# Kernel optimization log

Measured on AMD Instinct MI355X. Metric: run time of the kernel, lower is better.

The kernel has to match this reference:

```python
import jax, jax.numpy as jnp
import numpy as np

N_GO, N_KE, D = 8000, 2000, 16
N_LAYERS, N_TISSUE, DRUG = 3, 512, 2048
B = 256


def _scatter_add(msgs, dst, n):
    # msgs: [B, E, D] -> [B, n, D], summing messages into destination nodes
    Bm, _, d = msgs.shape
    return jnp.zeros((Bm, n, d), msgs.dtype).at[:, dst, :].add(msgs)


def setup_inputs() -> dict:
    key = jax.random.key(0)
    ks = jax.random.split(key, 20)
    inp = {
        "x": jax.random.normal(ks[0], (B, N_GO + DRUG), jnp.float32),
        "go_ke_src": jax.random.randint(ks[1], (50000,), 0, N_GO),
        "go_ke_dst": jax.random.randint(ks[2], (50000,), 0, N_KE),
        "ke_ke_src": jax.random.randint(ks[3], (20000,), 0, N_KE),
        "ke_ke_dst": jax.random.randint(ks[4], (20000,), 0, N_KE),
        "tissue": jax.random.randint(ks[5], (N_TISSUE,), 0, N_KE),
    }
    def w(k, shape, fan_in):
        return jax.random.normal(k, shape, jnp.float32) / np.sqrt(fan_in)
    inp["W_dec"] = w(ks[6], (N_GO, D), 1.0)          # per-GO scalar->vector layer
    inp["b_dec"] = jnp.zeros((N_GO, D), jnp.float32)
    inp["W_g2k"] = w(ks[7], (D, D), D)
    inp["b_g2k"] = jnp.zeros((D,), jnp.float32)
    inp["W_kk"] = w(ks[8], (N_LAYERS, D, D), D)
    inp["b_kk"] = jnp.zeros((N_LAYERS, D), jnp.float32)
    inp["w_ke"] = w(ks[9], (D,), D)                   # node readout D->1
    inp["b_ke"] = jnp.zeros((), jnp.float32)
    inp["W_bio1"] = w(ks[10], (N_TISSUE, 256), N_TISSUE)
    inp["b_bio1"] = jnp.zeros((256,), jnp.float32)
    inp["W_bio2"] = w(ks[11], (256, 128), 256)
    inp["b_bio2"] = jnp.zeros((128,), jnp.float32)
    inp["W_drug1"] = w(ks[12], (DRUG, 512), DRUG)
    inp["b_drug1"] = jnp.zeros((512,), jnp.float32)
    inp["W_drug2"] = w(ks[13], (512, 128), 512)
    inp["b_drug2"] = jnp.zeros((128,), jnp.float32)
    inp["W_pred"] = w(ks[14], (256, 1), 256)
    inp["b_pred"] = jnp.zeros((1,), jnp.float32)
    return inp


def reference(x, go_ke_src, go_ke_dst, ke_ke_src, ke_ke_dst, tissue,
              W_dec, b_dec, W_g2k, b_g2k, W_kk, b_kk, w_ke, b_ke,
              W_bio1, b_bio1, W_bio2, b_bio2,
              W_drug1, b_drug1, W_drug2, b_drug2, W_pred, b_pred):
    # go_decode_layer: per-GO scalar -> D-dim node feature
    go = jnp.tanh(x[:, :-DRUG, None] * W_dec + b_dec)          # [B, N_GO, D]
    # go2ke: gather source GO features, scatter-add into KE nodes, transform
    ke = _scatter_add(go[:, go_ke_src, :], go_ke_dst, N_KE)    # [B, N_KE, D]
    ke = jnp.tanh(ke @ W_g2k + b_g2k)
    # ke2ke message-passing layers
    for l in range(W_kk.shape[0]):
        agg = _scatter_add(ke[:, ke_ke_src, :], ke_ke_dst, N_KE)
        ke = jnp.tanh((ke + agg) @ W_kk[l] + b_kk[l])
    # ke_layer: per-node readout D -> scalar
    ke = jnp.tanh(jnp.einsum('bnd,d->bn', ke, w_ke) + b_ke)    # [B, N_KE]
    # tissue gather + bio MLP head
    bio = ke[:, tissue]                                         # [B, N_TISSUE]
    bio = jax.nn.relu(bio @ W_bio1 + b_bio1)
    bio = jax.nn.relu(bio @ W_bio2 + b_bio2)
    # drug fingerprint MLP head
    drug = x[:, -DRUG:]
    drug = jax.nn.relu(drug @ W_drug1 + b_drug1)
    drug = jax.nn.relu(drug @ W_drug2 + b_drug2)
    # predictor on concatenated features
    comb = jnp.concatenate([bio, drug], axis=-1)                # [B, 256]
    return comb @ W_pred + b_pred                               # [B, 1]
```

## Files before the change

### kernel.cpp

```cpp
#include <hip/hip_runtime.h>
#include <hip/hip_bf16.h>
#include <cstdint>
#include <cstddef>

#define BATCH 256
#define NGO   8000
#define NKE   2000
#define DD    16
#define XCOLS 10048
#define NDRUG 2048
#define NT    512
#define NSLAB 8
#define SB    32
#define TANH_SCALE 2.885390081777926f

__device__ __forceinline__ float tanh_fast(float z) {
    float e = __builtin_amdgcn_exp2f(z * TANH_SCALE);
    float r = __builtin_amdgcn_rcpf(e + 1.0f);
    return fmaf(-2.0f, r, 1.0f);
}

__device__ __forceinline__ float rcp_core(float zp) {
    float e = __builtin_amdgcn_exp2f(zp);
    return __builtin_amdgcn_rcpf(e + 1.0f);
}

__device__ __forceinline__ void add4(float4& a, const float4 b) {
    a.x += b.x; a.y += b.y; a.z += b.z; a.w += b.w;
}

#define RFL(v) __builtin_amdgcn_readfirstlane(v)

__global__ void k_scan2(const int* __restrict__ cnt_go, const int* __restrict__ cnt_kk,
                        int* __restrict__ rp_go, int* __restrict__ rp_kk) {
    const int* cnt = blockIdx.x ? cnt_kk : cnt_go;
    int* rowptr    = blockIdx.x ? rp_kk  : rp_go;
    __shared__ int s[2048];
    int t = threadIdx.x;
    s[t]        = (t        < NKE) ? cnt[t]        : 0;
    s[t + 1024] = (t + 1024 < NKE) ? cnt[t + 1024] : 0;
    __syncthreads();
    for (int st = 1; st < 2048; st <<= 1) {
        int v0 = (t >= st) ? s[t - st] : 0;
        int v1 = s[t + 1024 - st];
        __syncthreads();
        s[t] += v0; s[t + 1024] += v1;
        __syncthreads();
    }
    if (t == 0) rowptr[0] = 0;
    rowptr[t + 1] = s[t];
    if (t + 1024 < NKE) rowptr[t + 1025] = s[t + 1024];
}

__global__ void k_fill2(const int* __restrict__ gs, const int* __restrict__ gdst,
                        const int* __restrict__ ks, const int* __restrict__ kdst,
                        int Eg, int Ek,
                        const int* __restrict__ rp_go, int* __restrict__ cur_go, int* __restrict__ col_go,
                        const int* __restrict__ rp_kk, int* __restrict__ cur_kk, int* __restrict__ col_kk) {
    int e = blockIdx.x * 256 + threadIdx.x;
    if (e < Eg) {
        int d = gdst[e];
        int p = atomicAdd(&cur_go[d], 1);
        col_go[rp_go[d] + p] = gs[e];
    } else if (e < Eg + Ek) {
        int e2 = e - Eg;
        int d = kdst[e2];
        int p = atomicAdd(&cur_kk[d], 1);
        col_kk[rp_kk[d] + p] = ks[e2];
    }
}

__global__ __launch_bounds__(256) void k_prep(const float* __restrict__ x,
                                              float* __restrict__ xT,
                                              float* __restrict__ xdT,
                                              const float* __restrict__ bd,
                                              float* __restrict__ bds,
                                              const int* __restrict__ gdst,
                                              const int* __restrict__ kdst,
                                              int* __restrict__ cnt_go,
                                              int* __restrict__ cnt_kk,
                                              int Eg, int Ek) {
    int bid = blockIdx.x;
    if (bid >= 1128) {
        int e = (bid - 1128) * 256 + threadIdx.x;
        if (e < Eg) atomicAdd(&cnt_go[gdst[e]], 1);
        else if (e < Eg + Ek) atomicAdd(&cnt_kk[kdst[e - Eg]], 1);
        return;
    }
    if (bid >= 628) {
        int i = (bid - 628) * 256 + threadIdx.x;
        bds[i] = bd[i] * TANH_SCALE;
        return;
    }
    __shared__ float tile[64][69];
    int c4 = threadIdx.x & 15, rr = threadIdx.x >> 4;
    int n0, b0;
    bool isgo = bid < 500;
    if (isgo) { n0 = (bid % 125) * 64; b0 = (bid / 125) * 64; }
    else      { int t = bid - 500; n0 = NGO + (t & 31) * 64; b0 = (t >> 5) * 64; }
#pragma unroll
    for (int i = 0; i < 4; i++) {
        int row = rr + i * 16;
        float4 v = *(const float4*)&x[(size_t)(b0 + row) * XCOLS + n0 + c4 * 4];
        tile[row][c4 * 4 + 0] = v.x; tile[row][c4 * 4 + 1] = v.y;
        tile[row][c4 * 4 + 2] = v.z; tile[row][c4 * 4 + 3] = v.w;
    }
    __syncthreads();
#pragma unroll
    for (int i = 0; i < 4; i++) {
        int nrow = rr + i * 16;
        float4 w;
        w.x = tile[c4 * 4 + 0][nrow]; w.y = tile[c4 * 4 + 1][nrow];
        w.z = tile[c4 * 4 + 2][nrow]; w.w = tile[c4 * 4 + 3][nrow];
        if (isgo) {
            w.x *= TANH_SCALE; w.y *= TANH_SCALE; w.z *= TANH_SCALE; w.w *= TANH_SCALE;
            *(float4*)&xT[(size_t)(n0 + nrow) * 256 + b0 + c4 * 4] = w;
        } else {
            *(float4*)&xdT[(size_t)(n0 - NGO + nrow) * 256 + b0 + c4 * 4] = w;
        }
    }
}

__global__ __launch_bounds__(128) void k_fuse(const float* __restrict__ xT,
                                              const int* __restrict__ rowptr,
                                              const int* __restrict__ col,
                                              const float* __restrict__ Wd,
                                              const float* __restrict__ bds,
                                              const float* __restrict__ W,
                                              const float* __restrict__ bias,
                                              float* __restrict__ ke) {
    __shared__ float pre[32 * 17];
    __shared__ float Ws[256];
    __shared__ float bs[16];
    int s = blockIdx.x & 7, n = blockIdx.x >> 3;
    int tid = threadIdx.x;
    Ws[tid] = W[tid]; Ws[tid + 128] = W[tid + 128];
    if (tid < 16) bs[tid] = bias[tid];
    int bloc = tid >> 2, d4 = tid & 3;
    int bglob = s * SB + bloc;

    int e   = RFL(rowptr[n]);
    int end = RFL(rowptr[n + 1]);
    float degF = (float)(end - e);
    float4 acc = make_float4(0, 0, 0, 0);
    for (; e + 3 < end; e += 4) {
        int s0 = RFL(col[e]);
        int s1 = RFL(col[e + 1]);
        int s2 = RFL(col[e + 2]);
        int s3 = RFL(col[e + 3]);
        float xv0 = (xT + (size_t)s0 * 256)[bglob];
        float xv1 = (xT + (size_t)s1 * 256)[bglob];
        float xv2 = (xT + (size_t)s2 * 256)[bglob];
        float xv3 = (xT + (size_t)s3 * 256)[bglob];
        float4 w0 = *(const float4*)(Wd  + (size_t)s0 * 16 + d4 * 4);
        float4 w1 = *(const float4*)(Wd  + (size_t)s1 * 16 + d4 * 4);
        float4 w2 = *(const float4*)(Wd  + (size_t)s2 * 16 + d4 * 4);
        float4 w3 = *(const float4*)(Wd  + (size_t)s3 * 16 + d4 * 4);
        float4 c0 = *(const float4*)(bds + (size_t)s0 * 16 + d4 * 4);
        float4 c1 = *(const float4*)(bds + (size_t)s1 * 16 + d4 * 4);
        float4 c2 = *(const float4*)(bds + (size_t)s2 * 16 + d4 * 4);
        float4 c3 = *(const float4*)(bds + (size_t)s3 * 16 + d4 * 4);
        acc.x += rcp_core(fmaf(xv0, w0.x, c0.x)) + rcp_core(fmaf(xv1, w1.x, c1.x))
               + rcp_core(fmaf(xv2, w2.x, c2.x)) + rcp_core(fmaf(xv3, w3.x, c3.x));
        acc.y += rcp_core(fmaf(xv0, w0.y, c0.y)) + rcp_core(fmaf(xv1, w1.y, c1.y))
               + rcp_core(fmaf(xv2, w2.y, c2.y)) + rcp_core(fmaf(xv3, w3.y, c3.y));
        acc.z += rcp_core(fmaf(xv0, w0.z, c0.z)) + rcp_core(fmaf(xv1, w1.z, c1.z))
               + rcp_core(fmaf(xv2, w2.z, c2.z)) + rcp_core(fmaf(xv3, w3.z, c3.z));
        acc.w += rcp_core(fmaf(xv0, w0.w, c0.w)) + rcp_core(fmaf(xv1, w1.w, c1.w))
               + rcp_core(fmaf(xv2, w2.w, c2.w)) + rcp_core(fmaf(xv3, w3.w, c3.w));
    }
    for (; e < end; ++e) {
        int s0 = RFL(col[e]);
        float xv0 = (xT + (size_t)s0 * 256)[bglob];
        float4 w0 = *(const float4*)(Wd  + (size_t)s0 * 16 + d4 * 4);
        float4 c0 = *(const float4*)(bds + (size_t)s0 * 16 + d4 * 4);
        acc.x += rcp_core(fmaf(xv0, w0.x, c0.x));
        acc.y += rcp_core(fmaf(xv0, w0.y, c0.y));
        acc.z += rcp_core(fmaf(xv0, w0.z, c0.z));
        acc.w += rcp_core(fmaf(xv0, w0.w, c0.w));
    }
    pre[bloc * 17 + d4 * 4 + 0] = fmaf(-2.0f, acc.x, degF);
    pre[bloc * 17 + d4 * 4 + 1] = fmaf(-2.0f, acc.y, degF);
    pre[bloc * 17 + d4 * 4 + 2] = fmaf(-2.0f, acc.z, degF);
    pre[bloc * 17 + d4 * 4 + 3] = fmaf(-2.0f, acc.w, degF);
    __syncthreads();

    float4 o;
    float* op = &o.x;
#pragma unroll
    for (int q = 0; q < 4; q++) {
        int dp = d4 * 4 + q;
        float a = bs[dp];
#pragma unroll
        for (int d = 0; d < 16; d++) a = fmaf(pre[bloc * 17 + d], Ws[d * 16 + dp], a);
        op[q] = tanh_fast(a);
    }
    *(float4*)&ke[((size_t)s * NKE + n) * 512 + bloc * 16 + d4 * 4] = o;
}

__global__ __launch_bounds__(128) void k_layer(const float* __restrict__ kin,
                                               const int* __restrict__ rowptr,
                                               const int* __restrict__ col,
                                               const float* __restrict__ W,
                                               const float* __restrict__ bias,
                                               float* __restrict__ kout) {
    __shared__ float pre[32 * 17];
    __shared__ float Ws[256];
    __shared__ float bs[16];
    int s = blockIdx.x & 7, n = blockIdx.x >> 3;
    int tid = threadIdx.x;
    Ws[tid] = W[tid]; Ws[tid + 128] = W[tid + 128];
    if (tid < 16) bs[tid] = bias[tid];
    int bloc = tid >> 2, d4 = tid & 3;
    const float* slab = kin + (size_t)s * NKE * 512;

    float4 acc = *(const float4*)(slab + (size_t)n * 512 + tid * 4);
    int e   = RFL(rowptr[n]);
    int end = RFL(rowptr[n + 1]);
    for (; e + 3 < end; e += 4) {
        int c0 = RFL(col[e]), c1 = RFL(col[e + 1]), c2 = RFL(col[e + 2]), c3 = RFL(col[e + 3]);
        float4 v0 = *(const float4*)(slab + (size_t)c0 * 512 + tid * 4);
        float4 v1 = *(const float4*)(slab + (size_t)c1 * 512 + tid * 4);
        float4 v2 = *(const float4*)(slab + (size_t)c2 * 512 + tid * 4);
        float4 v3 = *(const float4*)(slab + (size_t)c3 * 512 + tid * 4);
        add4(acc, v0); add4(acc, v1); add4(acc, v2); add4(acc, v3);
    }
    for (; e < end; ++e) {
        int c0 = RFL(col[e]);
        float4 v0 = *(const float4*)(slab + (size_t)c0 * 512 + tid * 4);
        add4(acc, v0);
    }
    pre[bloc * 17 + d4 * 4 + 0] = acc.x;
    pre[bloc * 17 + d4 * 4 + 1] = acc.y;
    pre[bloc * 17 + d4 * 4 + 2] = acc.z;
    pre[bloc * 17 + d4 * 4 + 3] = acc.w;
    __syncthreads();

    float4 o;
    float* op = &o.x;
#pragma unroll
    for (int q = 0; q < 4; q++) {
        int dp = d4 * 4 + q;
        float a = bs[dp];
#pragma unroll
        for (int d = 0; d < 16; d++) a = fmaf(pre[bloc * 17 + d], Ws[d * 16 + dp], a);
        op[q] = tanh_fast(a);
    }
    *(float4*)&kout[(size_t)s * NKE * 512 + (size_t)n * 512 + bloc * 16 + d4 * 4] = o;
}

__device__ __forceinline__ void dev_kescalar(int t, const float* __restrict__ ke,
                                             const int* __restrict__ tissue,
                                             const float* __restrict__ wke,
                                             const float* __restrict__ bke,
                                             float* __restrict__ bioT) {
    int b = threadIdx.x;
    int n = RFL(tissue[t]);
    int s = b >> 5, bloc = b & 31;
    const float4* kp = (const float4*)&ke[((size_t)s * NKE + n) * 512 + bloc * 16];
    const float4* wp = (const float4*)wke;
    float4 k0 = kp[0], k1 = kp[1], k2 = kp[2], k3 = kp[3];
    float4 w0 = wp[0], w1 = wp[1], w2 = wp[2], w3 = wp[3];
    float acc = bke[0];
    acc += k0.x * w0.x + k0.y * w0.y + k0.z * w0.z + k0.w * w0.w;
    acc += k1.x * w1.x + k1.y * w1.y + k1.z * w1.z + k1.w * w1.w;
    acc += k2.x * w2.x + k2.y * w2.y + k2.z * w2.z + k2.w * w2.w;
    acc += k3.x * w3.x + k3.y * w3.y + k3.z * w3.z + k3.w * w3.w;
    bioT[t * 256 + b] = tanh_fast(acc);
}

__device__ __forceinline__ void dev_gemm(int bid, const float* __restrict__ A,
                                         const float* __restrict__ W,
                                         float* __restrict__ Cpart,
                                         int N, int Kper, int gx,
                                         float (*As)[68], float (*Ws)[68]) {
    int tid = threadIdx.x;
    int tx = tid & 15, ty = tid >> 4;
    int jx = bid % gx;
    int by = (bid / gx) & 3;
    int ks = bid / (gx * 4);
    int jt = jx * 64, bt = by * 64;
    int k0 = ks * Kper;

    float acc[4][4];
#pragma unroll
    for (int i = 0; i < 4; i++)
#pragma unroll
        for (int j = 0; j < 4; j++) acc[i][j] = 0.0f;

    for (int kc = 0; kc < Kper; kc += 32) {
#pragma unroll
        for (int i = 0; i < 8; i++) {
            int idx = tid + i * 256;
            int kk = idx >> 6, cc = idx & 63;
            As[kk][cc] = A[(size_t)(k0 + kc + kk) * 256 + bt + cc];
            Ws[kk][cc] = W[(size_t)(k0 + kc + kk) * N + jt + cc];
        }
        __syncthreads();
#pragma unroll 8
        for (int kk = 0; kk < 32; kk++) {
            float4 a = *(const float4*)&As[kk][tx * 4];
            float4 w = *(const float4*)&Ws[kk][ty * 4];
            acc[0][0] = fmaf(w.x, a.x, acc[0][0]); acc[0][1] = fmaf(w.x, a.y, acc[0][1]);
            acc[0][2] = fmaf(w.x, a.z, acc[0][2]); acc[0][3] = fmaf(w.x, a.w, acc[0][3]);
            acc[1][0] = fmaf(w.y, a.x, acc[1][0]); acc[1][1] = fmaf(w.y, a.y, acc[1][1]);
            acc[1][2] = fmaf(w.y, a.z, acc[1][2]); acc[1][3] = fmaf(w.y, a.w, acc[1][3]);
            acc[2][0] = fmaf(w.z, a.x, acc[2][0]); acc[2][1] = fmaf(w.z, a.y, acc[2][1]);
            acc[2][2] = fmaf(w.z, a.z, acc[2][2]); acc[2][3] = fmaf(w.z, a.w, acc[2][3]);
            acc[3][0] = fmaf(w.w, a.x, acc[3][0]); acc[3][1] = fmaf(w.w, a.y, acc[3][1]);
            acc[3][2] = fmaf(w.w, a.z, acc[3][2]); acc[3][3] = fmaf(w.w, a.w, acc[3][3]);
        }
        __syncthreads();
    }
#pragma unroll
    for (int jy = 0; jy < 4; jy++) {
        int j = jt + ty * 4 + jy;
        float4 v = make_float4(acc[jy][0], acc[jy][1], acc[jy][2], acc[jy][3]);
        *(float4*)&Cpart[((size_t)ks * N + j) * 256 + bt + tx * 4] = v;
    }
}

__device__ __forceinline__ void dev_red(int j, const float* __restrict__ Cpart,
                                        const float* __restrict__ bias,
                                        float* __restrict__ C, int N, int S) {
    int b = threadIdx.x;
    float acc = bias[j];
    for (int s = 0; s < S; s++) acc += Cpart[((size_t)s * N + j) * 256 + b];
    C[j * 256 + b] = fmaxf(acc, 0.0f);
}

__global__ __launch_bounds__(256) void k_kg(const float* __restrict__ ke,
                                            const int* __restrict__ tissue,
                                            const float* __restrict__ wke,
                                            const float* __restrict__ bke,
                                            float* __restrict__ bioT,
                                            const float* __restrict__ A,
                                            const float* __restrict__ W,
                                            float* __restrict__ Cpart,
                                            int N, int Kper, int gx, int nk) {
    __shared__ float As[32][68];
    __shared__ float Ws[32][68];
    int bid = blockIdx.x;
    if (bid < nk) dev_kescalar(bid, ke, tissue, wke, bke, bioT);
    else          dev_gemm(bid - nk, A, W, Cpart, N, Kper, gx, As, Ws);
}

__global__ __launch_bounds__(256) void k_gr(const float* __restrict__ A,
                                            const float* __restrict__ W,
                                            float* __restrict__ Cpart,
                                            int N, int Kper, int gx, int gB,
                                            const float* __restrict__ Rcp,
                                            const float* __restrict__ Rbias,
                                            float* __restrict__ RC, int RN, int RS) {
    __shared__ float As[32][68];
    __shared__ float Ws[32][68];
    int bid = blockIdx.x;
    if (bid < gB) dev_gemm(bid, A, W, Cpart, N, Kper, gx, As, Ws);
    else          dev_red(bid - gB, Rcp, Rbias, RC, RN, RS);
}

__global__ __launch_bounds__(256) void k_red(const float* __restrict__ Cpart,
                                             const float* __restrict__ bias,
                                             float* __restrict__ C, int N, int S) {
    dev_red(blockIdx.x, Cpart, bias, C, N, S);
}

__global__ __launch_bounds__(256) void k_final(const float* __restrict__ bio2T,
                                               const float* __restrict__ drug2T,
                                               const float* __restrict__ Wp,
                                               const float* __restrict__ bp,
                                               float* __restrict__ out) {
    int b = threadIdx.x;
    float acc = bp[0];
#pragma unroll 8
    for (int i = 0; i < 128; i++) acc = fmaf(bio2T[i * 256 + b], Wp[i], acc);
#pragma unroll 8
    for (int i = 0; i < 128; i++) acc = fmaf(drug2T[i * 256 + b], Wp[128 + i], acc);
    out[b] = acc;
}

extern "C" void kernel_launch(void* const* d_in, const int* in_sizes, int n_in,
                              void* d_out, int out_size, void* d_ws, size_t ws_size,
                              hipStream_t stream) {
    const float* x       = (const float*)d_in[0];
    const int*   go_src  = (const int*)d_in[1];
    const int*   go_dst  = (const int*)d_in[2];
    const int*   kk_src  = (const int*)d_in[3];
    const int*   kk_dst  = (const int*)d_in[4];
    const int*   tissue  = (const int*)d_in[5];
    const float* W_dec   = (const float*)d_in[6];
    const float* b_dec   = (const float*)d_in[7];
    const float* W_g2k   = (const float*)d_in[8];
    const float* b_g2k   = (const float*)d_in[9];
    const float* W_kk    = (const float*)d_in[10];
    const float* b_kk    = (const float*)d_in[11];
    const float* w_ke    = (const float*)d_in[12];
    const float* b_ke    = (const float*)d_in[13];
    const float* W_bio1  = (const float*)d_in[14];
    const float* b_bio1  = (const float*)d_in[15];
    const float* W_bio2  = (const float*)d_in[16];
    const float* b_bio2  = (const float*)d_in[17];
    const float* W_drug1 = (const float*)d_in[18];
    const float* b_drug1 = (const float*)d_in[19];
    const float* W_drug2 = (const float*)d_in[20];
    const float* b_drug2 = (const float*)d_in[21];
    const float* W_pred  = (const float*)d_in[22];
    const float* b_pred  = (const float*)d_in[23];
    float* out = (float*)d_out;

    const int E_GO = in_sizes[1];
    const int E_KK = in_sizes[3];

    char* wsb = (char*)d_ws;
    size_t off = 0;
    float* xT      = (float*)(wsb + off); off += (size_t)NGO * 256 * 4;
    float* ke_a    = (float*)(wsb + off); off += (size_t)NSLAB * NKE * 512 * 4;
    float* ke_b    = (float*)(wsb + off); off += (size_t)NSLAB * NKE * 512 * 4;
    float* bio_inT = (float*)(wsb + off); off += (size_t)NT * 256 * 4;
    float* bio1T   = (float*)(wsb + off); off += (size_t)256 * 256 * 4;
    float* bio2T   = (float*)(wsb + off); off += (size_t)128 * 256 * 4;
    float* xdT     = (float*)(wsb + off); off += (size_t)NDRUG * 256 * 4;
    float* drug1T  = (float*)(wsb + off); off += (size_t)512 * 256 * 4;
    float* drug2T  = (float*)(wsb + off); off += (size_t)128 * 256 * 4;
    float* bds     = (float*)(wsb + off); off += (size_t)NGO * 16 * 4;
    float* cp_d1   = (float*)(wsb + off); off += (size_t)8 * 512 * 256 * 4;
    float* cp_b1   = (float*)(wsb + off); off += (size_t)8 * 256 * 256 * 4;
    float* cp_d2   = (float*)(wsb + off); off += (size_t)8 * 128 * 256 * 4;
    float* cp_b2   = (float*)(wsb + off); off += (size_t)8 * 128 * 256 * 4;
    int* cnt_go    = (int*)(wsb + off); off += 2048 * 4;
    int* cur_go    = (int*)(wsb + off); off += 2048 * 4;
    int* cnt_kk    = (int*)(wsb + off); off += 2048 * 4;
    int* cur_kk    = (int*)(wsb + off); off += 2048 * 4;
    int* rp_go     = (int*)(wsb + off); off += 2048 * 4;
    int* rp_kk     = (int*)(wsb + off); off += 2048 * 4;
    int* col_go    = (int*)(wsb + off); off += 50048 * 4;
    int* col_kk    = (int*)(wsb + off); off += 20048 * 4;

    hipMemsetAsync(cnt_go, 0, 4 * 2048 * 4, stream);

    int Etot = E_GO + E_KK;
    int histBlocks = (Etot + 255) / 256;

    k_prep<<<1128 + histBlocks, 256, 0, stream>>>(x, xT, xdT, b_dec, bds,
                                                  go_dst, kk_dst, cnt_go, cnt_kk, E_GO, E_KK);
    k_scan2<<<2, 1024, 0, stream>>>(cnt_go, cnt_kk, rp_go, rp_kk);
    k_fill2<<<histBlocks, 256, 0, stream>>>(go_src, go_dst, kk_src, kk_dst, E_GO, E_KK,
                                            rp_go, cur_go, col_go, rp_kk, cur_kk, col_kk);

    k_fuse<<<NKE * NSLAB, 128, 0, stream>>>(xT, rp_go, col_go, W_dec, bds, W_g2k, b_g2k, ke_a);
    k_layer<<<NKE * NSLAB, 128, 0, stream>>>(ke_a, rp_kk, col_kk, W_kk + 0 * 256, b_kk + 0 * 16, ke_b);
    k_layer<<<NKE * NSLAB, 128, 0, stream>>>(ke_b, rp_kk, col_kk, W_kk + 1 * 256, b_kk + 1 * 16, ke_a);
    k_layer<<<NKE * NSLAB, 128, 0, stream>>>(ke_a, rp_kk, col_kk, W_kk + 2 * 256, b_kk + 2 * 16, ke_b);

    k_kg<<<NT + 256, 256, 0, stream>>>(ke_b, tissue, w_ke, b_ke, bio_inT,
                                       xdT, W_drug1, cp_d1, 512, 256, 8, NT);
    k_gr<<<128 + 512, 256, 0, stream>>>(bio_inT, W_bio1, cp_b1, 256, 64, 4, 128,
                                        cp_d1, b_drug1, drug1T, 512, 8);
    k_gr<<<64 + 256, 256, 0, stream>>>(drug1T, W_drug2, cp_d2, 128, 64, 2, 64,
                                       cp_b1, b_bio1, bio1T, 256, 8);
    k_gr<<<64 + 128, 256, 0, stream>>>(bio1T, W_bio2, cp_b2, 128, 32, 2, 64,
                                       cp_d2, b_drug2, drug2T, 128, 8);
    k_red<<<128, 256, 0, stream>>>(cp_b2, b_bio2, bio2T, 128, 8);

    k_final<<<1, 256, 0, stream>>>(bio2T, drug2T, W_pred, b_pred, out);
}
```

Before: 222.1 us.

## Gather neighbor KE features in fp16 and pair sigmoid terms to share reciprocals

Each KE layer kernel now also writes an fp16 copy of its output, and the next layer gathers neighbor features from that half-width copy. This halves the bytes moved by the random neighbor gathers, while the self term still reads fp32. In the GO-to-KE kernel, two sigmoid-style terms are combined algebraically so that one reciprocal is computed per pair instead of two. The costs are an extra fp16 store per layer, reduced precision in the aggregated messages, and possible overflow in the product of two exponentials for large inputs.

```diff
diff --git a/kernel.cpp b/kernel.cpp
--- a/kernel.cpp
+++ b/kernel.cpp
@@ -13,6 +13,8 @@
 #define NSLAB 8
 #define SB    32
 #define TANH_SCALE 2.885390081777926f
+
+typedef __attribute__((ext_vector_type(4))) _Float16 half4;
 
 __device__ __forceinline__ float tanh_fast(float z) {
     float e = __builtin_amdgcn_exp2f(z * TANH_SCALE);
@@ -128,7 +130,8 @@
                                               const float* __restrict__ bds,
                                               const float* __restrict__ W,
                                               const float* __restrict__ bias,
-                                              float* __restrict__ ke) {
+                                              float* __restrict__ ke,
+                                              _Float16* __restrict__ keH) {
     __shared__ float pre[32 * 17];
     __shared__ float Ws[256];
     __shared__ float bs[16];
@@ -143,33 +146,45 @@
     int end = RFL(rowptr[n + 1]);
     float degF = (float)(end - e);
     float4 acc = make_float4(0, 0, 0, 0);
-    for (; e + 3 < end; e += 4) {
+    for (; e + 1 < end; e += 2) {
         int s0 = RFL(col[e]);
         int s1 = RFL(col[e + 1]);
-        int s2 = RFL(col[e + 2]);
-        int s3 = RFL(col[e + 3]);
         float xv0 = (xT + (size_t)s0 * 256)[bglob];
         float xv1 = (xT + (size_t)s1 * 256)[bglob];
-        float xv2 = (xT + (size_t)s2 * 256)[bglob];
-        float xv3 = (xT + (size_t)s3 * 256)[bglob];
         float4 w0 = *(const float4*)(Wd  + (size_t)s0 * 16 + d4 * 4);
+        float4 c0 = *(const float4*)(bds + (size_t)s0 * 16 + d4 * 4);
         float4 w1 = *(const float4*)(Wd  + (size_t)s1 * 16 + d4 * 4);
-        float4 w2 = *(const float4*)(Wd  + (size_t)s2 * 16 + d4 * 4);
-        float4 w3 = *(const float4*)(Wd  + (size_t)s3 * 16 + d4 * 4);
-        float4 c0 = *(const float4*)(bds + (size_t)s0 * 16 + d4 * 4);
         float4 c1 = *(const float4*)(bds + (size_t)s1 * 16 + d4 * 4);
-        float4 c2 = *(const float4*)(bds + (size_t)s2 * 16 + d4 * 4);
-        float4 c3 = *(const float4*)(bds + (size_t)s3 * 16 + d4 * 4);
-        acc.x += rcp_core(fmaf(xv0, w0.x, c0.x)) + rcp_core(fmaf(xv1, w1.x, c1.x))
-               + rcp_core(fmaf(xv2, w2.x, c2.x)) + rcp_core(fmaf(xv3, w3.x, c3.x));
-        acc.y += rcp_core(fmaf(xv0, w0.y, c0.y)) + rcp_core(fmaf(xv1, w1.y, c1.y))
-               + rcp_core(fmaf(xv2, w2.y, c2.y)) + rcp_core(fmaf(xv3, w3.y, c3.y));
-        acc.z += rcp_core(fmaf(xv0, w0.z, c0.z)) + rcp_core(fmaf(xv1, w1.z, c1.z))
-               + rcp_core(fmaf(xv2, w2.z, c2.z)) + rcp_core(fmaf(xv3, w3.z, c3.z));
-        acc.w += rcp_core(fmaf(xv0, w0.w, c0.w)) + rcp_core(fmaf(xv1, w1.w, c1.w))
-               + rcp_core(fmaf(xv2, w2.w, c2.w)) + rcp_core(fmaf(xv3, w3.w, c3.w));
-    }
-    for (; e < end; ++e) {
+        {
+            float e0x = __builtin_amdgcn_exp2f(fmaf(xv0, w0.x, c0.x));
+            float e1x = __builtin_amdgcn_exp2f(fmaf(xv1, w1.x, c1.x));
+            float sx = e0x + e1x;
+            float den = fmaf(e0x, e1x, sx + 1.0f);
+            acc.x = fmaf(sx + 2.0f, __builtin_amdgcn_rcpf(den), acc.x);
+        }
+        {
+            float e0x = __builtin_amdgcn_exp2f(fmaf(xv0, w0.y, c0.y));
+            float e1x = __builtin_amdgcn_exp2f(fmaf(xv1, w1.y, c1.y));
+            float sx = e0x + e1x;
+            float den = fmaf(e0x, e1x, sx + 1.0f);
+            acc.y = fmaf(sx + 2.0f, __builtin_amdgcn_rcpf(den), acc.y);
+        }
+        {
+            float e0x = __builtin_amdgcn_exp2f(fmaf(xv0, w0.z, c0.z));
+            float e1x = __builtin_amdgcn_exp2f(fmaf(xv1, w1.z, c1.z));
+            float sx = e0x + e1x;
+            float den = fmaf(e0x, e1x, sx + 1.0f);
+            acc.z = fmaf(sx + 2.0f, __builtin_amdgcn_rcpf(den), acc.z);
+        }
+        {
+            float e0x = __builtin_amdgcn_exp2f(fmaf(xv0, w0.w, c0.w));
+            float e1x = __builtin_amdgcn_exp2f(fmaf(xv1, w1.w, c1.w));
+            float sx = e0x + e1x;
+            float den = fmaf(e0x, e1x, sx + 1.0f);
+            acc.w = fmaf(sx + 2.0f, __builtin_amdgcn_rcpf(den), acc.w);
+        }
+    }
+    if (e < end) {
         int s0 = RFL(col[e]);
         float xv0 = (xT + (size_t)s0 * 256)[bglob];
         float4 w0 = *(const float4*)(Wd  + (size_t)s0 * 16 + d4 * 4);
@@ -195,15 +210,21 @@
         for (int d = 0; d < 16; d++) a = fmaf(pre[bloc * 17 + d], Ws[d * 16 + dp], a);
         op[q] = tanh_fast(a);
     }
-    *(float4*)&ke[((size_t)s * NKE + n) * 512 + bloc * 16 + d4 * 4] = o;
+    size_t base = ((size_t)s * NKE + n) * 512 + bloc * 16 + d4 * 4;
+    *(float4*)&ke[base] = o;
+    half4 hv;
+    hv[0] = (_Float16)o.x; hv[1] = (_Float16)o.y; hv[2] = (_Float16)o.z; hv[3] = (_Float16)o.w;
+    *(half4*)&keH[base] = hv;
 }
 
 __global__ __launch_bounds__(128) void k_layer(const float* __restrict__ kin,
+                                               const _Float16* __restrict__ kinH,
                                                const int* __restrict__ rowptr,
                                                const int* __restrict__ col,
                                                const float* __restrict__ W,
                                                const float* __restrict__ bias,
-                                               float* __restrict__ kout) {
+                                               float* __restrict__ kout,
+                                               _Float16* __restrict__ koutH) {
     __shared__ float pre[32 * 17];
     __shared__ float Ws[256];
     __shared__ float bs[16];
@@ -212,23 +233,26 @@
     Ws[tid] = W[tid]; Ws[tid + 128] = W[tid + 128];
     if (tid < 16) bs[tid] = bias[tid];
     int bloc = tid >> 2, d4 = tid & 3;
-    const float* slab = kin + (size_t)s * NKE * 512;
+    const float*    slab  = kin  + (size_t)s * NKE * 512;
+    const _Float16* slabH = kinH + (size_t)s * NKE * 512;
 
     float4 acc = *(const float4*)(slab + (size_t)n * 512 + tid * 4);
     int e   = RFL(rowptr[n]);
     int end = RFL(rowptr[n + 1]);
-    for (; e + 3 < end; e += 4) {
-        int c0 = RFL(col[e]), c1 = RFL(col[e + 1]), c2 = RFL(col[e + 2]), c3 = RFL(col[e + 3]);
-        float4 v0 = *(const float4*)(slab + (size_t)c0 * 512 + tid * 4);
-        float4 v1 = *(const float4*)(slab + (size_t)c1 * 512 + tid * 4);
-        float4 v2 = *(const float4*)(slab + (size_t)c2 * 512 + tid * 4);
-        float4 v3 = *(const float4*)(slab + (size_t)c3 * 512 + tid * 4);
-        add4(acc, v0); add4(acc, v1); add4(acc, v2); add4(acc, v3);
-    }
-    for (; e < end; ++e) {
+    for (; e + 1 < end; e += 2) {
+        int c0 = RFL(col[e]), c1 = RFL(col[e + 1]);
+        half4 v0 = *(const half4*)(slabH + (size_t)c0 * 512 + tid * 4);
+        half4 v1 = *(const half4*)(slabH + (size_t)c1 * 512 + tid * 4);
+        acc.x += (float)v0[0] + (float)v1[0];
+        acc.y += (float)v0[1] + (float)v1[1];
+        acc.z += (float)v0[2] + (float)v1[2];
+        acc.w += (float)v0[3] + (float)v1[3];
+    }
+    if (e < end) {
         int c0 = RFL(col[e]);
-        float4 v0 = *(const float4*)(slab + (size_t)c0 * 512 + tid * 4);
-        add4(acc, v0);
+        half4 v0 = *(const half4*)(slabH + (size_t)c0 * 512 + tid * 4);
+        acc.x += (float)v0[0]; acc.y += (float)v0[1];
+        acc.z += (float)v0[2]; acc.w += (float)v0[3];
     }
     pre[bloc * 17 + d4 * 4 + 0] = acc.x;
     pre[bloc * 17 + d4 * 4 + 1] = acc.y;
@@ -246,7 +270,11 @@
         for (int d = 0; d < 16; d++) a = fmaf(pre[bloc * 17 + d], Ws[d * 16 + dp], a);
         op[q] = tanh_fast(a);
     }
-    *(float4*)&kout[(size_t)s * NKE * 512 + (size_t)n * 512 + bloc * 16 + d4 * 4] = o;
+    size_t base = ((size_t)s * NKE + n) * 512 + bloc * 16 + d4 * 4;
+    *(float4*)&kout[base] = o;
+    half4 hv;
+    hv[0] = (_Float16)o.x; hv[1] = (_Float16)o.y; hv[2] = (_Float16)o.z; hv[3] = (_Float16)o.w;
+    *(half4*)&koutH[base] = hv;
 }
 
 __device__ __forceinline__ void dev_kescalar(int t, const float* __restrict__ ke,
@@ -416,6 +444,8 @@
     float* xT      = (float*)(wsb + off); off += (size_t)NGO * 256 * 4;
     float* ke_a    = (float*)(wsb + off); off += (size_t)NSLAB * NKE * 512 * 4;
     float* ke_b    = (float*)(wsb + off); off += (size_t)NSLAB * NKE * 512 * 4;
+    _Float16* keH_a = (_Float16*)(wsb + off); off += (size_t)NSLAB * NKE * 512 * 2;
+    _Float16* keH_b = (_Float16*)(wsb + off); off += (size_t)NSLAB * NKE * 512 * 2;
     float* bio_inT = (float*)(wsb + off); off += (size_t)NT * 256 * 4;
     float* bio1T   = (float*)(wsb + off); off += (size_t)256 * 256 * 4;
     float* bio2T   = (float*)(wsb + off); off += (size_t)128 * 256 * 4;
@@ -447,10 +477,14 @@
     k_fill2<<<histBlocks, 256, 0, stream>>>(go_src, go_dst, kk_src, kk_dst, E_GO, E_KK,
                                             rp_go, cur_go, col_go, rp_kk, cur_kk, col_kk);
 
-    k_fuse<<<NKE * NSLAB, 128, 0, stream>>>(xT, rp_go, col_go, W_dec, bds, W_g2k, b_g2k, ke_a);
-    k_layer<<<NKE * NSLAB, 128, 0, stream>>>(ke_a, rp_kk, col_kk, W_kk + 0 * 256, b_kk + 0 * 16, ke_b);
-    k_layer<<<NKE * NSLAB, 128, 0, stream>>>(ke_b, rp_kk, col_kk, W_kk + 1 * 256, b_kk + 1 * 16, ke_a);
-    k_layer<<<NKE * NSLAB, 128, 0, stream>>>(ke_a, rp_kk, col_kk, W_kk + 2 * 256, b_kk + 2 * 16, ke_b);
+    k_fuse<<<NKE * NSLAB, 128, 0, stream>>>(xT, rp_go, col_go, W_dec, bds, W_g2k, b_g2k,
+                                            ke_a, keH_a);
+    k_layer<<<NKE * NSLAB, 128, 0, stream>>>(ke_a, keH_a, rp_kk, col_kk,
+                                             W_kk + 0 * 256, b_kk + 0 * 16, ke_b, keH_b);
+    k_layer<<<NKE * NSLAB, 128, 0, stream>>>(ke_b, keH_b, rp_kk, col_kk,
+                                             W_kk + 1 * 256, b_kk + 1 * 16, ke_a, keH_a);
+    k_layer<<<NKE * NSLAB, 128, 0, stream>>>(ke_a, keH_a, rp_kk, col_kk,
+                                             W_kk + 2 * 256, b_kk + 2 * 16, ke_b, keH_b);
 
     k_kg<<<NT + 256, 256, 0, stream>>>(ke_b, tissue, w_ke, b_ke, bio_inT,
                                        xdT, W_drug1, cp_d1, 512, 256, 8, NT);
```

Result: no change. 225.6 us (+1.5%).
